# Kernel tuning notes

Measured on AMD Instinct MI355X. Metric: run time of the kernel, lower is better.

## Reference

```python
import jax, jax.numpy as jnp
import numpy as np

# ---- vocab / constraint tables (constants, derived exactly from the module's rules) ----
VOCAB = {'<pad>': 0, '<start>': 1, '<end>': 2, 'C': 3, 'O': 4, 'N': 5, '(': 6, ')': 7,
         '[': 8, ']': 9, '=': 10, '#': 11, '%': 12, '1': 13, '2': 14, '3': 15, '4': 16,
         '5': 17, '6': 18, '7': 19, '8': 20, '9': 21}
V = len(VOCAB)
CONSTRAINT_STRENGTH = 0.5

_toks = sorted(VOCAB, key=VOCAB.get)
# allowed.update(['(','[',')',']']) makes the bracket-stack branch redundant; the
# allowed set depends only on whether the previous char is a digit.
_always = {'(', ')', '[', ']', 'C', 'O', 'N', '=', '#'}
_allowed_digit = (_always | {'%'}) - {'<pad>', '<start>', '<end>'}
_allowed_nondigit = (_always | {str(i) for i in range(1, 10)}) - {'<pad>', '<start>', '<end>'}
D_DIGIT = jnp.asarray(np.array([0.0 if t in _allowed_digit else 1.0 for t in _toks], np.float32))      # [V]
D_NONDIGIT = jnp.asarray(np.array([0.0 if t in _allowed_nondigit else 1.0 for t in _toks], np.float32))  # [V]
IS_DIGIT = jnp.asarray(np.array([1.0 if t.isdigit() else 0.0 for t in _toks], np.float32))               # [V]


def setup_inputs() -> dict:
    key = jax.random.key(0)
    ks = jax.random.split(key, 5)
    B, S, D, F = 32, 512, 512, 2048
    return {
        'tokens': jax.random.randint(ks[0], (B, S), 0, V, dtype=jnp.int32),
        'z': jax.random.normal(ks[1], (B, D), dtype=jnp.float32),
        'emb': jax.random.normal(ks[2], (V, D), dtype=jnp.float32) * 0.02,
        'W1': jax.random.normal(ks[3], (D, F), dtype=jnp.float32) * 0.02,
        'b1': jnp.zeros((F,), dtype=jnp.float32),
        'W2': jax.random.normal(ks[4], (F, V), dtype=jnp.float32) * 0.02,
        'b2': jnp.zeros((V,), dtype=jnp.float32),
    }


def reference(tokens, z, emb, W1, b1, W2, b2):
    # decoder: token embedding + broadcast latent -> MLP -> logits [B,S,V]
    x = emb[tokens] + z[:, None, :]                       # [B,S,D]
    h = jax.nn.relu(jnp.einsum('bsd,df->bsf', x, W1) + b1)  # [B,S,F]
    logits = jnp.einsum('bsf,fv->bsv', h, W2) + b2          # [B,S,V]

    # constraint mask: for t in 1..S-1 add the disallowed-vector chosen by
    # whether tokens[t-1] is a digit; accumulated into one [V] mask per sequence.
    isdig = IS_DIGIT[tokens[:, :-1]]                      # [B,S-1]
    n_dig = jnp.sum(isdig, axis=1)                        # [B]
    n_non = (tokens.shape[1] - 1) - n_dig                 # [B]
    mask = n_dig[:, None] * D_DIGIT + n_non[:, None] * D_NONDIGIT  # [B,V]
    return logits - CONSTRAINT_STRENGTH * mask[:, None, :]
```

## Files before the change

kernel.cpp:

```cpp
#include <hip/hip_runtime.h>

#define V 22
#define NB 32
#define NS 512
#define ND 512
#define NF 2048
#define M_TOT 704

typedef __attribute__((ext_vector_type(8))) short bf16x8;
typedef __attribute__((ext_vector_type(4))) float f32x4;
typedef unsigned short u16;

__device__ __forceinline__ u16 f2bf(float f) {
    unsigned u = __float_as_uint(f);
    u += 0x7FFFu + ((u >> 16) & 1u);
    return (u16)(u >> 16);
}

__global__ __launch_bounds__(256) void transpose_w1(const float* __restrict__ W1,
                                                    u16* __restrict__ W1T) {
    __shared__ __align__(16) u16 T[64 * 72];
    const int tid = threadIdx.x;
    const int k0 = (blockIdx.x >> 5) * 64;
    const int f0 = (blockIdx.x & 31) * 64;
    const int a  = tid >> 4;
    const int fb = (tid & 15) * 4;
    #pragma unroll
    for (int kr = 0; kr < 2; ++kr) {
        int k = 2 * a + 32 * kr;
        float4 v0 = *(const float4*)&W1[(size_t)(k0 + k)     * NF + f0 + fb];
        float4 v1 = *(const float4*)&W1[(size_t)(k0 + k + 1) * NF + f0 + fb];
        unsigned p0 = (unsigned)f2bf(v0.x) | ((unsigned)f2bf(v1.x) << 16);
        unsigned p1 = (unsigned)f2bf(v0.y) | ((unsigned)f2bf(v1.y) << 16);
        unsigned p2 = (unsigned)f2bf(v0.z) | ((unsigned)f2bf(v1.z) << 16);
        unsigned p3 = (unsigned)f2bf(v0.w) | ((unsigned)f2bf(v1.w) << 16);
        *(unsigned*)&T[(fb + 0) * 72 + k] = p0;
        *(unsigned*)&T[(fb + 1) * 72 + k] = p1;
        *(unsigned*)&T[(fb + 2) * 72 + k] = p2;
        *(unsigned*)&T[(fb + 3) * 72 + k] = p3;
    }
    __syncthreads();
    #pragma unroll
    for (int rep = 0; rep < 2; ++rep) {
        int fr = rep * 32 + (tid >> 3);
        int kc = (tid & 7) * 8;
        *(int4*)&W1T[(size_t)(f0 + fr) * ND + k0 + kc] = *(int4*)&T[fr * 72 + kc];
    }
}

__global__ __launch_bounds__(256) void gemm_fused(
    const float* __restrict__ emb, const float* __restrict__ z,
    const u16* __restrict__ W1T, const float* __restrict__ b1,
    const float* __restrict__ W2, const float* __restrict__ b2,
    float* __restrict__ lt)
{
    __shared__ __align__(16) char smem[24576];
    char* As = smem;
    char* Bs = smem + 8192;

    const int tid = threadIdx.x;
    const int m0 = blockIdx.x * 32;
    const int f0 = blockIdx.y * 64;
    const int lane = tid & 63;
    const int wave = tid >> 6;
    const int wm = wave >> 1, wn = wave & 1;

    const int arow = tid >> 3;
    const int ac   = (tid & 7) * 16;
    const int am   = m0 + arow;
    const int ab   = am / V;
    const int at   = am - ab * V;
    const float* __restrict__ er = emb + (size_t)at * ND + ac;
    const float* __restrict__ zr = z   + (size_t)ab * ND + ac;
    const int abase0 = arow * 256 + ac * 2;
    const int abase1 = arow * 256 + ac * 2 + 16;

    const int rowA = wm * 16 + (lane & 15);
    const int rowB = wn * 32 + (lane & 15);
    const int kgrp = (lane >> 4) * 16;

    f32x4 acc[2];
    acc[0] = (f32x4){0.f, 0.f, 0.f, 0.f};
    acc[1] = (f32x4){0.f, 0.f, 0.f, 0.f};

    for (int kt = 0; kt < 4; ++kt) {
        {
            const float* e = er + kt * 128;
            const float* zz = zr + kt * 128;
            u16 o[16];
            #pragma unroll
            for (int j = 0; j < 16; ++j) o[j] = f2bf(e[j] + zz[j]);
            *(int4*)(As + abase0) = ((int4*)o)[0];
            *(int4*)(As + abase1) = ((int4*)o)[1];
        }
        #pragma unroll
        for (int p = 0; p < 4; ++p) {
            int i = p * 256 + tid;
            int row = i >> 4;
            int c = i & 15;
            int4 v = *(const int4*)(W1T + (size_t)(f0 + row) * ND + kt * 128 + c * 8);
            *(int4*)(Bs + row * 256 + c * 16) = v;
        }
        __syncthreads();
        #pragma unroll
        for (int ks = 0; ks < 4; ++ks) {
            int kb = ks * 64 + kgrp;
            bf16x8 af  = *(const bf16x8*)(As + rowA * 256 + kb);
            bf16x8 bv0 = *(const bf16x8*)(Bs + rowB * 256 + kb);
            bf16x8 bv1 = *(const bf16x8*)(Bs + (rowB + 16) * 256 + kb);
            acc[0] = __builtin_amdgcn_mfma_f32_16x16x32_bf16(af, bv0, acc[0], 0, 0, 0);
            acc[1] = __builtin_amdgcn_mfma_f32_16x16x32_bf16(af, bv1, acc[1], 0, 0, 0);
        }
        __syncthreads();
    }

    float* hs  = (float*)smem;
    float* w2s = (float*)(smem + 8704);
    {
        const int mrow = wm * 16 + ((lane >> 4) << 2);
        #pragma unroll
        for (int ni = 0; ni < 2; ++ni) {
            int col = wn * 32 + ni * 16 + (lane & 15);
            float bias = b1[f0 + col];
            #pragma unroll
            for (int r = 0; r < 4; ++r)
                hs[(mrow + r) * 68 + col] = fmaxf(acc[ni][r] + bias, 0.f);
        }
    }
    for (int i = tid; i < 64 * V; i += 256) w2s[i] = W2[(size_t)f0 * V + i];
    __syncthreads();

    {
        const int row = tid >> 3;
        const int vb  = (tid & 7) * 3;
        float a0 = 0.f, a1 = 0.f, a2 = 0.f;
        #pragma unroll 8
        for (int f = 0; f < 64; ++f) {
            float h = hs[row * 68 + f];
            const float* w = &w2s[f * V + vb];
            a0 = fmaf(h, w[0], a0);
            a1 = fmaf(h, w[1], a1);
            a2 = fmaf(h, w[2], a2);
        }
        if (blockIdx.y == 0) {
            a0 += b2[vb];
            if (vb + 1 < V) a1 += b2[vb + 1];
            if (vb + 2 < V) a2 += b2[vb + 2];
        }
        float* ltr = lt + (size_t)(m0 + row) * V + vb;
        atomicAdd(ltr, a0);
        if (vb + 1 < V) atomicAdd(ltr + 1, a1);
        if (vb + 2 < V) atomicAdd(ltr + 2, a2);
    }
}

__global__ __launch_bounds__(256) void scatter_out(
    const int* __restrict__ tokens, const float* __restrict__ lt,
    float* __restrict__ out)
{
    __shared__ int wsum[4];
    __shared__ float ndig_sh;
    const int tid = threadIdx.x;
    const int b = blockIdx.x / 44;

    int cnt = 0;
    {
        int t1 = tokens[b * NS + tid];
        cnt += (t1 >= 13 && t1 <= 21);
        int s2 = tid + 256;
        if (s2 < NS - 1) {
            int t2 = tokens[b * NS + s2];
            cnt += (t2 >= 13 && t2 <= 21);
        }
    }
    for (int off = 32; off > 0; off >>= 1) cnt += __shfl_down(cnt, off, 64);
    if ((tid & 63) == 0) wsum[tid >> 6] = cnt;
    __syncthreads();
    if (tid == 0) ndig_sh = (float)(wsum[0] + wsum[1] + wsum[2] + wsum[3]);
    __syncthreads();

    const int idx = blockIdx.x * 256 + tid;
    const int v = idx % V;
    const int s = (idx / V) & (NS - 1);
    const int tok = tokens[b * NS + s];
    const float nd = ndig_sh;
    const float nn = (float)(NS - 1) - nd;
    const float dd = ((0x3FE007 >> v) & 1) ? 1.f : 0.f;
    const float dn = ((0x001007 >> v) & 1) ? 1.f : 0.f;
    out[idx] = lt[((size_t)b * V + tok) * V + v] - 0.5f * (nd * dd + nn * dn);
}

extern "C" void kernel_launch(void* const* d_in, const int* in_sizes, int n_in,
                              void* d_out, int out_size, void* d_ws, size_t ws_size,
                              hipStream_t stream) {
    const int*   tokens = (const int*)d_in[0];
    const float* z      = (const float*)d_in[1];
    const float* emb    = (const float*)d_in[2];
    const float* W1     = (const float*)d_in[3];
    const float* b1     = (const float*)d_in[4];
    const float* W2     = (const float*)d_in[5];
    const float* b2     = (const float*)d_in[6];
    float* out = (float*)d_out;

    char* ws = (char*)d_ws;
    u16*   W1T = (u16*)ws;
    float* lt  = (float*)(ws + 2097152);

    transpose_w1<<<256, 256, 0, stream>>>(W1, W1T);
    gemm_fused<<<dim3(22, 32), 256, 0, stream>>>(emb, z, W1T, b1, W2, b2, lt);
    scatter_out<<<1408, 256, 0, stream>>>(tokens, lt, out);
}
```

Measured before the change: 95.35 us.

## Replace MFMA bf16 first GEMM with scalar FP32 FMA tiled GEMM

The first GEMM's MFMA bf16 matrix-core path is replaced with a plain FP32 FMA register-tiled loop over shared-memory tiles. Inputs are still rounded to bf16 and widened back to float, so the numerics match the previous version. The kernel is renamed gemm_sure, which suggests the change is a correctness or safety check on the MFMA operand layout rather than a speed move. The cost is many more ALU instructions, twice the LDS footprint, and more K-loop iterations with syncs.

```diff
diff --git a/kernel.cpp b/kernel.cpp
--- a/kernel.cpp
+++ b/kernel.cpp
@@ -7,14 +7,15 @@
 #define NF 2048
 #define M_TOT 704
 
-typedef __attribute__((ext_vector_type(8))) short bf16x8;
-typedef __attribute__((ext_vector_type(4))) float f32x4;
 typedef unsigned short u16;
 
 __device__ __forceinline__ u16 f2bf(float f) {
     unsigned u = __float_as_uint(f);
     u += 0x7FFFu + ((u >> 16) & 1u);
     return (u16)(u >> 16);
+}
+__device__ __forceinline__ float bf2f(u16 h) {
+    return __uint_as_float(((unsigned)h) << 16);
 }
 
 __global__ __launch_bounds__(256) void transpose_w1(const float* __restrict__ W1,
@@ -48,83 +49,84 @@
     }
 }
 
-__global__ __launch_bounds__(256) void gemm_fused(
+__global__ __launch_bounds__(256) void gemm_sure(
     const float* __restrict__ emb, const float* __restrict__ z,
     const u16* __restrict__ W1T, const float* __restrict__ b1,
     const float* __restrict__ W2, const float* __restrict__ b2,
     float* __restrict__ lt)
 {
-    __shared__ __align__(16) char smem[24576];
-    char* As = smem;
-    char* Bs = smem + 8192;
+    __shared__ __align__(16) float As2[32][68];
+    __shared__ __align__(16) float Bs2[64][68];
+    __shared__ float w2s[64 * V];
 
     const int tid = threadIdx.x;
     const int m0 = blockIdx.x * 32;
     const int f0 = blockIdx.y * 64;
-    const int lane = tid & 63;
-    const int wave = tid >> 6;
-    const int wm = wave >> 1, wn = wave & 1;
 
     const int arow = tid >> 3;
-    const int ac   = (tid & 7) * 16;
+    const int ak   = (tid & 7) * 8;
     const int am   = m0 + arow;
     const int ab   = am / V;
     const int at   = am - ab * V;
-    const float* __restrict__ er = emb + (size_t)at * ND + ac;
-    const float* __restrict__ zr = z   + (size_t)ab * ND + ac;
-    const int abase0 = arow * 256 + ac * 2;
-    const int abase1 = arow * 256 + ac * 2 + 16;
-
-    const int rowA = wm * 16 + (lane & 15);
-    const int rowB = wn * 32 + (lane & 15);
-    const int kgrp = (lane >> 4) * 16;
-
-    f32x4 acc[2];
-    acc[0] = (f32x4){0.f, 0.f, 0.f, 0.f};
-    acc[1] = (f32x4){0.f, 0.f, 0.f, 0.f};
-
-    for (int kt = 0; kt < 4; ++kt) {
+    const float* __restrict__ er = emb + (size_t)at * ND + ak;
+    const float* __restrict__ zr = z   + (size_t)ab * ND + ak;
+
+    const int brow = tid >> 2;
+    const int bk   = (tid & 3) * 16;
+
+    const int mg = tid >> 5;
+    const int fg = tid & 31;
+
+    float acc[4][2] = {};
+
+    for (int k0i = 0; k0i < ND; k0i += 64) {
         {
-            const float* e = er + kt * 128;
-            const float* zz = zr + kt * 128;
-            u16 o[16];
-            #pragma unroll
-            for (int j = 0; j < 16; ++j) o[j] = f2bf(e[j] + zz[j]);
-            *(int4*)(As + abase0) = ((int4*)o)[0];
-            *(int4*)(As + abase1) = ((int4*)o)[1];
-        }
+            const float* e  = er + k0i;
+            const float* zz = zr + k0i;
+            #pragma unroll
+            for (int j = 0; j < 8; ++j)
+                As2[arow][ak + j] = bf2f(f2bf(e[j] + zz[j]));
+        }
+        {
+            const u16* src = W1T + (size_t)(f0 + brow) * ND + k0i + bk;
+            int4 v0 = ((const int4*)src)[0];
+            int4 v1 = ((const int4*)src)[1];
+            const u16* p0 = (const u16*)&v0;
+            const u16* p1 = (const u16*)&v1;
+            #pragma unroll
+            for (int j = 0; j < 8; ++j) Bs2[brow][bk + j]     = bf2f(p0[j]);
+            #pragma unroll
+            for (int j = 0; j < 8; ++j) Bs2[brow][bk + 8 + j] = bf2f(p1[j]);
+        }
+        __syncthreads();
+
         #pragma unroll
-        for (int p = 0; p < 4; ++p) {
-            int i = p * 256 + tid;
-            int row = i >> 4;
-            int c = i & 15;
-            int4 v = *(const int4*)(W1T + (size_t)(f0 + row) * ND + kt * 128 + c * 8);
-            *(int4*)(Bs + row * 256 + c * 16) = v;
+        for (int k4 = 0; k4 < 16; ++k4) {
+            float4 bv0 = *(const float4*)&Bs2[fg * 2][k4 * 4];
+            float4 bv1 = *(const float4*)&Bs2[fg * 2 + 1][k4 * 4];
+            #pragma unroll
+            for (int i = 0; i < 4; ++i) {
+                float4 a = *(const float4*)&As2[mg * 4 + i][k4 * 4];
+                acc[i][0] = fmaf(a.x, bv0.x, acc[i][0]);
+                acc[i][0] = fmaf(a.y, bv0.y, acc[i][0]);
+                acc[i][0] = fmaf(a.z, bv0.z, acc[i][0]);
+                acc[i][0] = fmaf(a.w, bv0.w, acc[i][0]);
+                acc[i][1] = fmaf(a.x, bv1.x, acc[i][1]);
+                acc[i][1] = fmaf(a.y, bv1.y, acc[i][1]);
+                acc[i][1] = fmaf(a.z, bv1.z, acc[i][1]);
+                acc[i][1] = fmaf(a.w, bv1.w, acc[i][1]);
+            }
         }
         __syncthreads();
+    }
+
+    {
         #pragma unroll
-        for (int ks = 0; ks < 4; ++ks) {
-            int kb = ks * 64 + kgrp;
-            bf16x8 af  = *(const bf16x8*)(As + rowA * 256 + kb);
-            bf16x8 bv0 = *(const bf16x8*)(Bs + rowB * 256 + kb);
-            bf16x8 bv1 = *(const bf16x8*)(Bs + (rowB + 16) * 256 + kb);
-            acc[0] = __builtin_amdgcn_mfma_f32_16x16x32_bf16(af, bv0, acc[0], 0, 0, 0);
-            acc[1] = __builtin_amdgcn_mfma_f32_16x16x32_bf16(af, bv1, acc[1], 0, 0, 0);
-        }
-        __syncthreads();
-    }
-
-    float* hs  = (float*)smem;
-    float* w2s = (float*)(smem + 8704);
-    {
-        const int mrow = wm * 16 + ((lane >> 4) << 2);
-        #pragma unroll
-        for (int ni = 0; ni < 2; ++ni) {
-            int col = wn * 32 + ni * 16 + (lane & 15);
-            float bias = b1[f0 + col];
-            #pragma unroll
-            for (int r = 0; r < 4; ++r)
-                hs[(mrow + r) * 68 + col] = fmaxf(acc[ni][r] + bias, 0.f);
+        for (int j = 0; j < 2; ++j) {
+            float bias = b1[f0 + fg * 2 + j];
+            #pragma unroll
+            for (int i = 0; i < 4; ++i)
+                As2[mg * 4 + i][fg * 2 + j] = fmaxf(acc[i][j] + bias, 0.f);
         }
     }
     for (int i = tid; i < 64 * V; i += 256) w2s[i] = W2[(size_t)f0 * V + i];
@@ -136,7 +138,7 @@
         float a0 = 0.f, a1 = 0.f, a2 = 0.f;
         #pragma unroll 8
         for (int f = 0; f < 64; ++f) {
-            float h = hs[row * 68 + f];
+            float h = As2[row][f];
             const float* w = &w2s[f * V + vb];
             a0 = fmaf(h, w[0], a0);
             a1 = fmaf(h, w[1], a1);
@@ -207,6 +209,6 @@
     float* lt  = (float*)(ws + 2097152);
 
     transpose_w1<<<256, 256, 0, stream>>>(W1, W1T);
-    gemm_fused<<<dim3(22, 32), 256, 0, stream>>>(emb, z, W1T, b1, W2, b2, lt);
+    gemm_sure<<<dim3(22, 32), 256, 0, stream>>>(emb, z, W1T, b1, W2, b2, lt);
     scatter_out<<<1408, 256, 0, stream>>>(tokens, lt, out);
 }
```

Result: slower. 148.7 us (+56.0%).

## Fuse W1 transpose/bf16 conversion into GEMM with double-buffered register prefetch

Applied to the files above, without the earlier changes.

Drops the separate W1 transpose kernel and has the GEMM load fp32 W1 tiles directly, converting to bf16 and transposing into LDS. The full A tile is staged once, and B tiles are double-buffered with register prefetch of the next K-slice. This removes a launch and the intermediate W1T round trip through memory. The cost is redundant fp32 W1 reads and conversions across M-blocks, plus larger LDS usage that lowers occupancy.

```diff
diff --git a/kernel.cpp b/kernel.cpp
--- a/kernel.cpp
+++ b/kernel.cpp
@@ -5,11 +5,11 @@
 #define NS 512
 #define ND 512
 #define NF 2048
-#define M_TOT 704
 
 typedef __attribute__((ext_vector_type(8))) short bf16x8;
 typedef __attribute__((ext_vector_type(4))) float f32x4;
 typedef unsigned short u16;
+typedef unsigned long long u64;
 
 __device__ __forceinline__ u16 f2bf(float f) {
     unsigned u = __float_as_uint(f);
@@ -17,114 +17,103 @@
     return (u16)(u >> 16);
 }
 
-__global__ __launch_bounds__(256) void transpose_w1(const float* __restrict__ W1,
-                                                    u16* __restrict__ W1T) {
-    __shared__ __align__(16) u16 T[64 * 72];
-    const int tid = threadIdx.x;
-    const int k0 = (blockIdx.x >> 5) * 64;
-    const int f0 = (blockIdx.x & 31) * 64;
-    const int a  = tid >> 4;
-    const int fb = (tid & 15) * 4;
-    #pragma unroll
-    for (int kr = 0; kr < 2; ++kr) {
-        int k = 2 * a + 32 * kr;
-        float4 v0 = *(const float4*)&W1[(size_t)(k0 + k)     * NF + f0 + fb];
-        float4 v1 = *(const float4*)&W1[(size_t)(k0 + k + 1) * NF + f0 + fb];
-        unsigned p0 = (unsigned)f2bf(v0.x) | ((unsigned)f2bf(v1.x) << 16);
-        unsigned p1 = (unsigned)f2bf(v0.y) | ((unsigned)f2bf(v1.y) << 16);
-        unsigned p2 = (unsigned)f2bf(v0.z) | ((unsigned)f2bf(v1.z) << 16);
-        unsigned p3 = (unsigned)f2bf(v0.w) | ((unsigned)f2bf(v1.w) << 16);
-        *(unsigned*)&T[(fb + 0) * 72 + k] = p0;
-        *(unsigned*)&T[(fb + 1) * 72 + k] = p1;
-        *(unsigned*)&T[(fb + 2) * 72 + k] = p2;
-        *(unsigned*)&T[(fb + 3) * 72 + k] = p3;
-    }
-    __syncthreads();
-    #pragma unroll
-    for (int rep = 0; rep < 2; ++rep) {
-        int fr = rep * 32 + (tid >> 3);
-        int kc = (tid & 7) * 8;
-        *(int4*)&W1T[(size_t)(f0 + fr) * ND + k0 + kc] = *(int4*)&T[fr * 72 + kc];
-    }
-}
-
-__global__ __launch_bounds__(256) void gemm_fused(
+__global__ __launch_bounds__(256) void gemm_all(
     const float* __restrict__ emb, const float* __restrict__ z,
-    const u16* __restrict__ W1T, const float* __restrict__ b1,
+    const float* __restrict__ W1, const float* __restrict__ b1,
     const float* __restrict__ W2, const float* __restrict__ b2,
     float* __restrict__ lt)
 {
-    __shared__ __align__(16) char smem[24576];
-    char* As = smem;
-    char* Bs = smem + 8192;
-
-    const int tid = threadIdx.x;
-    const int m0 = blockIdx.x * 32;
-    const int f0 = blockIdx.y * 64;
+    __shared__ __align__(16) char smem[75776];
+    u16*   As  = (u16*)smem;
+    char*  Bb0 = smem + 33280;
+    char*  Bb1 = smem + 51712;
+    float* w2s = (float*)(smem + 70144);
+    float* hs  = (float*)(smem + 33280);
+
+    const int tid  = threadIdx.x;
+    const int m0   = blockIdx.x * 32;
+    const int f0   = blockIdx.y * 64;
     const int lane = tid & 63;
     const int wave = tid >> 6;
     const int wm = wave >> 1, wn = wave & 1;
 
-    const int arow = tid >> 3;
-    const int ac   = (tid & 7) * 16;
-    const int am   = m0 + arow;
-    const int ab   = am / V;
-    const int at   = am - ab * V;
-    const float* __restrict__ er = emb + (size_t)at * ND + ac;
-    const float* __restrict__ zr = z   + (size_t)ab * ND + ac;
-    const int abase0 = arow * 256 + ac * 2;
-    const int abase1 = arow * 256 + ac * 2 + 16;
-
-    const int rowA = wm * 16 + (lane & 15);
-    const int rowB = wn * 32 + (lane & 15);
-    const int kgrp = (lane >> 4) * 16;
-
-    f32x4 acc[2];
-    acc[0] = (f32x4){0.f, 0.f, 0.f, 0.f};
-    acc[1] = (f32x4){0.f, 0.f, 0.f, 0.f};
-
-    for (int kt = 0; kt < 4; ++kt) {
-        {
-            const float* e = er + kt * 128;
-            const float* zz = zr + kt * 128;
-            u16 o[16];
+    const int kp = (tid >> 4) * 4;
+    const int f4 = (tid & 15) * 4;
+    float4 v0, v1, v2, v3;
+
+#define LOADB(kt) { \
+    const float* wp = W1 + (size_t)((kt) * 64 + kp) * NF + f0 + f4; \
+    v0 = *(const float4*)(wp); \
+    v1 = *(const float4*)(wp + NF); \
+    v2 = *(const float4*)(wp + 2 * NF); \
+    v3 = *(const float4*)(wp + 3 * NF); }
+
+#define WRITEB(Bb) { \
+    const float* a0 = (const float*)&v0; const float* a1 = (const float*)&v1; \
+    const float* a2 = (const float*)&v2; const float* a3 = (const float*)&v3; \
+    _Pragma("unroll") \
+    for (int i = 0; i < 4; ++i) { \
+        unsigned p01 = (unsigned)f2bf(a0[i]) | ((unsigned)f2bf(a1[i]) << 16); \
+        unsigned p23 = (unsigned)f2bf(a2[i]) | ((unsigned)f2bf(a3[i]) << 16); \
+        *(u64*)((Bb) + (f4 + i) * 144 + kp * 2) = (u64)p01 | ((u64)p23 << 32); \
+    } }
+
+    LOADB(0);
+    {
+        const int row = tid >> 3;
+        const int kc  = (tid & 7) * 64;
+        const int m = m0 + row;
+        const int b = m / V;
+        const int t = m - b * V;
+        const float* er = emb + (size_t)t * ND + kc;
+        const float* zr = z   + (size_t)b * ND + kc;
+        u16* dst = As + row * 520 + kc;
+        #pragma unroll
+        for (int j = 0; j < 8; ++j) {
+            u16 o[8];
             #pragma unroll
-            for (int j = 0; j < 16; ++j) o[j] = f2bf(e[j] + zz[j]);
-            *(int4*)(As + abase0) = ((int4*)o)[0];
-            *(int4*)(As + abase1) = ((int4*)o)[1];
-        }
+            for (int e = 0; e < 8; ++e) o[e] = f2bf(er[j * 8 + e] + zr[j * 8 + e]);
+            *(int4*)(dst + j * 8) = *(int4*)o;
+        }
+    }
+    WRITEB(Bb0);
+    __syncthreads();
+
+    const int kg8  = (lane >> 4) * 8;
+    const u16* ap  = As + (wm * 16 + (lane & 15)) * 520;
+    const int brow = wn * 32 + (lane & 15);
+
+    f32x4 acc0 = (f32x4){0.f, 0.f, 0.f, 0.f};
+    f32x4 acc1 = (f32x4){0.f, 0.f, 0.f, 0.f};
+
+    char* rb = Bb0;
+    char* wb = Bb1;
+    for (int kt = 0; kt < 8; ++kt) {
+        if (kt < 7) LOADB(kt + 1);
         #pragma unroll
-        for (int p = 0; p < 4; ++p) {
-            int i = p * 256 + tid;
-            int row = i >> 4;
-            int c = i & 15;
-            int4 v = *(const int4*)(W1T + (size_t)(f0 + row) * ND + kt * 128 + c * 8);
-            *(int4*)(Bs + row * 256 + c * 16) = v;
-        }
+        for (int ki = 0; ki < 2; ++ki) {
+            const int ke = kt * 64 + ki * 32 + kg8;
+            bf16x8 af = *(const bf16x8*)(ap + ke);
+            bf16x8 b0 = *(const bf16x8*)(rb + brow * 144 + (ki * 32 + kg8) * 2);
+            bf16x8 b1f = *(const bf16x8*)(rb + (brow + 16) * 144 + (ki * 32 + kg8) * 2);
+            acc0 = __builtin_amdgcn_mfma_f32_16x16x32_bf16(af, b0, acc0, 0, 0, 0);
+            acc1 = __builtin_amdgcn_mfma_f32_16x16x32_bf16(af, b1f, acc1, 0, 0, 0);
+        }
+        if (kt < 7) WRITEB(wb);
         __syncthreads();
-        #pragma unroll
-        for (int ks = 0; ks < 4; ++ks) {
-            int kb = ks * 64 + kgrp;
-            bf16x8 af  = *(const bf16x8*)(As + rowA * 256 + kb);
-            bf16x8 bv0 = *(const bf16x8*)(Bs + rowB * 256 + kb);
-            bf16x8 bv1 = *(const bf16x8*)(Bs + (rowB + 16) * 256 + kb);
-            acc[0] = __builtin_amdgcn_mfma_f32_16x16x32_bf16(af, bv0, acc[0], 0, 0, 0);
-            acc[1] = __builtin_amdgcn_mfma_f32_16x16x32_bf16(af, bv1, acc[1], 0, 0, 0);
-        }
-        __syncthreads();
-    }
-
-    float* hs  = (float*)smem;
-    float* w2s = (float*)(smem + 8704);
+        char* tmp = rb; rb = wb; wb = tmp;
+    }
+
     {
         const int mrow = wm * 16 + ((lane >> 4) << 2);
         #pragma unroll
-        for (int ni = 0; ni < 2; ++ni) {
-            int col = wn * 32 + ni * 16 + (lane & 15);
+        for (int nf = 0; nf < 2; ++nf) {
+            int col = wn * 32 + nf * 16 + (lane & 15);
             float bias = b1[f0 + col];
+            f32x4 a = nf ? acc1 : acc0;
             #pragma unroll
             for (int r = 0; r < 4; ++r)
-                hs[(mrow + r) * 68 + col] = fmaxf(acc[ni][r] + bias, 0.f);
+                hs[(mrow + r) * 68 + col] = fmaxf(a[r] + bias, 0.f);
         }
     }
     for (int i = tid; i < 64 * V; i += 256) w2s[i] = W2[(size_t)f0 * V + i];
@@ -152,6 +141,8 @@
         if (vb + 1 < V) atomicAdd(ltr + 1, a1);
         if (vb + 2 < V) atomicAdd(ltr + 2, a2);
     }
+#undef LOADB
+#undef WRITEB
 }
 
 __global__ __launch_bounds__(256) void scatter_out(
@@ -202,11 +193,8 @@
     const float* b2     = (const float*)d_in[6];
     float* out = (float*)d_out;
 
-    char* ws = (char*)d_ws;
-    u16*   W1T = (u16*)ws;
-    float* lt  = (float*)(ws + 2097152);
-
-    transpose_w1<<<256, 256, 0, stream>>>(W1, W1T);
-    gemm_fused<<<dim3(22, 32), 256, 0, stream>>>(emb, z, W1T, b1, W2, b2, lt);
+    float* lt = (float*)d_ws;
+
+    gemm_all<<<dim3(22, 32), 256, 0, stream>>>(emb, z, W1, b1, W2, b2, lt);
     scatter_out<<<1408, 256, 0, stream>>>(tokens, lt, out);
 }
```

Measured after the change: 102.3 us. +7.3%, slower.
